# Performance work log

Measured on AMD Instinct MI355X. Metric: run time of the kernel, lower is better.

## Reference

```python
import jax, jax.numpy as jnp
import numpy as np

KS = 3                      # kernel side
GRID_SIZE = 5
SPLINE_ORDER = 3
N_CONVS = 8
IN_FEAT = KS * KS           # KANLinear in_features per patch
NCOEF = GRID_SIZE + SPLINE_ORDER  # number of B-spline basis functions


def setup_inputs() -> dict:
    key = jax.random.key(0)
    k1, k2, k3, k4 = jax.random.split(key, 4)
    x = jax.random.normal(k1, (8, 32, 64, 64), jnp.float32)
    # efficient-kan KANLinear params, stacked over the n_convs independent kernels
    base_weight = jax.random.normal(k2, (N_CONVS, IN_FEAT), jnp.float32) / np.sqrt(IN_FEAT).astype(np.float32)
    spline_weight = jax.random.normal(k3, (N_CONVS, IN_FEAT, NCOEF), jnp.float32) * 0.1
    spline_scaler = jax.random.normal(k4, (N_CONVS, IN_FEAT), jnp.float32) / np.sqrt(IN_FEAT).astype(np.float32)
    # knot grid: uniform over grid_range=[-1,1], extended by spline_order on each side
    h = 2.0 / GRID_SIZE
    g = jnp.arange(-SPLINE_ORDER, GRID_SIZE + SPLINE_ORDER + 1, dtype=jnp.float32) * h - 1.0
    grid = jnp.tile(g[None, :], (IN_FEAT, 1))  # [in, G+2k+1]
    return {"x": x, "base_weight": base_weight, "spline_weight": spline_weight,
            "spline_scaler": spline_scaler, "grid": grid}


def b_splines(x, grid):
    # x: [..., in], grid: [in, G+2k+1] -> bases [..., in, G+k]  (Cox-de Boor)
    xe = x[..., None]
    bases = ((xe >= grid[:, :-1]) & (xe < grid[:, 1:])).astype(x.dtype)
    for k in range(1, SPLINE_ORDER + 1):
        left = (xe - grid[:, :-(k + 1)]) / (grid[:, k:-1] - grid[:, :-(k + 1)])
        right = (grid[:, k + 1:] - xe) / (grid[:, k + 1:] - grid[:, 1:-k])
        bases = left * bases[..., :-1] + right * bases[..., 1:]
    return bases


def reference(x, base_weight, spline_weight, spline_scaler, grid):
    B, C, H, W = x.shape
    ho, wo = H - KS + 1, W - KS + 1  # stride 1, dilation 1, no padding
    # im2col: [B, C*KS*KS, ho, wo], channel-major feature order (matches torch Unfold)
    patches = jax.lax.conv_general_dilated_patches(x, (KS, KS), (1, 1), 'VALID')
    patches = patches.reshape(B, C, IN_FEAT, ho * wo).transpose(0, 1, 3, 2)  # [B,C,L,in]
    # KANLinear(out_features=1) applied per conv n over each patch
    base = jnp.einsum('bcli,ni->bcnl', jax.nn.silu(patches), base_weight)
    basis = b_splines(patches, grid)                     # [B,C,L,in,coef]
    sw = spline_weight * spline_scaler[..., None]        # scaled spline weight [n,in,coef]
    spl = jnp.einsum('bclis,nis->bcnl', basis, sw)
    # output channel index = kern + channel * n_convs (channel-major)
    return (base + spl).reshape(B, C * N_CONVS, ho, wo)
```

## Files before the change

kernel.cpp:

```cpp
#include <hip/hip_runtime.h>
#include <hip/hip_bf16.h>

#define N_CONVS 8
#define IN_FEAT 9
#define NCOEF 8
#define NKNOT 12
#define HH 64
#define WW 64
#define HO 62
#define WO 62
#define BAND 16
#define LROWS 18
#define LW 67


__global__ __launch_bounds__(704) void kan_prep(const float* __restrict__ bw,
                                                const float* __restrict__ sw,
                                                const float* __restrict__ sc,
                                                const float* __restrict__ grid,
                                                float* __restrict__ cbuf) {
    int t = threadIdx.x;
    if (t < 648) {
        int j = t % 9, ni = t / 9;
        cbuf[t] = (j == 0) ? bw[ni] : sw[ni * 8 + (j - 1)] * sc[ni];
    } else if (t < 659) {
        int j = t - 648; cbuf[t] = 1.0f / (grid[j + 1] - grid[j]);
    } else if (t < 669) {
        int j = t - 659; cbuf[t] = 1.0f / (grid[j + 2] - grid[j]);
    } else if (t < 678) {
        int j = t - 669; cbuf[t] = 1.0f / (grid[j + 3] - grid[j]);
    }
}

__global__ __launch_bounds__(256, 3) void kan_main(const float* __restrict__ x,
                                                   const float* __restrict__ grid,
                                                   const float* __restrict__ cbuf,
                                                   float* __restrict__ out) {
    __shared__ float feat[LROWS * LW * 9];

    const int blk  = blockIdx.x;
    const int band = blk & 3;
    const int img  = blk >> 2;
    const int r0   = band * BAND;
    const int nr       = (HO - r0) < BAND ? (HO - r0) : BAND;
    const int nrows_in = (HH - r0) < LROWS ? (HH - r0) : LROWS;

    float g[NKNOT];
#pragma unroll
    for (int j = 0; j < NKNOT; j++) g[j] = grid[j];
    float i1[11], i2[10], i3[9];
#pragma unroll
    for (int j = 0; j < 11; j++) i1[j] = cbuf[648 + j];
#pragma unroll
    for (int j = 0; j < 10; j++) i2[j] = cbuf[659 + j];
#pragma unroll
    for (int j = 0; j < 9; j++)  i3[j] = cbuf[669 + j];

    const float* xb = x + (size_t)img * (HH * WW) + (size_t)r0 * WW;
    for (int p = threadIdx.x; p < nrows_in * WW; p += 256) {
        const int r = p >> 6, c = p & 63;
        const float xv = xb[r * WW + c];

        const float sg = 1.0f / (1.0f + expf(-xv));
        const float s0 = xv * sg;

        float ee[12], d[12];
#pragma unroll
        for (int j = 0; j < 12; j++) {
            ee[j] = xv - g[j];
            d[j]  = (xv >= g[j]) ? 1.0f : 0.0f;
        }
        float b0[11];
#pragma unroll
        for (int j = 0; j < 11; j++) b0[j] = d[j] - d[j + 1];
        float b1[10];
#pragma unroll
        for (int j = 0; j < 10; j++)
            b1[j] = (ee[j] * i1[j]) * b0[j] - (ee[j + 2] * i1[j + 1]) * b0[j + 1];
        float b2[9];
#pragma unroll
        for (int j = 0; j < 9; j++)
            b2[j] = (ee[j] * i2[j]) * b1[j] - (ee[j + 3] * i2[j + 1]) * b1[j + 1];
        float b3[8];
#pragma unroll
        for (int j = 0; j < 8; j++)
            b3[j] = (ee[j] * i3[j]) * b2[j] - (ee[j + 4] * i3[j + 1]) * b2[j + 1];

        float* f = &feat[(r * LW + c) * 9];
        f[0] = s0;
#pragma unroll
        for (int j = 0; j < 8; j++) f[j + 1] = b3[j];
    }
    __syncthreads();

    const int row = threadIdx.x >> 4;
    const int xs  = (threadIdx.x & 15) * 4;
    if (row < nr) {
        float acc[N_CONVS][4];
#pragma unroll
        for (int n = 0; n < N_CONVS; n++)
#pragma unroll
            for (int t = 0; t < 4; t++) acc[n][t] = 0.0f;

#pragma unroll 1
        for (int ky = 0; ky < 3; ky++) {
            float fw[6][9];
#pragma unroll
            for (int c6 = 0; c6 < 6; c6++) {
                const float* fp = &feat[((row + ky) * LW + xs + c6) * 9];
#pragma unroll
                for (int j = 0; j < 9; j++) fw[c6][j] = fp[j];
            }
#pragma unroll
            for (int kx = 0; kx < 3; kx++) {
#pragma unroll
                for (int n = 0; n < N_CONVS; n++) {
#pragma unroll
                    for (int j = 0; j < 9; j++) {
                        const float w = cbuf[((n * 9) + (ky * 3 + kx)) * 9 + j];
#pragma unroll
                        for (int t = 0; t < 4; t++)
                            acc[n][t] = fmaf(fw[kx + t][j], w, acc[n][t]);
                    }
                }
            }
        }

        const int oy = r0 + row;
        float* ob = out + ((size_t)img * N_CONVS) * (HO * WO) + oy * WO + xs;
#pragma unroll
        for (int n = 0; n < N_CONVS; n++) {
            float* o = ob + n * (HO * WO);
            *(float2*)o = make_float2(acc[n][0], acc[n][1]);
            if (xs < 58) *(float2*)(o + 2) = make_float2(acc[n][2], acc[n][3]);
        }
    }
}

extern "C" void kernel_launch(void* const* d_in, const int* in_sizes, int n_in,
                              void* d_out, int out_size, void* d_ws, size_t ws_size,
                              hipStream_t stream) {
    const float* x    = (const float*)d_in[0];
    const float* bw   = (const float*)d_in[1];
    const float* sw   = (const float*)d_in[2];
    const float* sc   = (const float*)d_in[3];
    const float* grid = (const float*)d_in[4];
    float* out  = (float*)d_out;
    float* cbuf = (float*)d_ws;

    kan_prep<<<1, 704, 0, stream>>>(bw, sw, sc, grid, cbuf);
    kan_main<<<256 * 4, 256, 0, stream>>>(x, grid, cbuf, out);
}
```

Baseline: 95.48 us.

## Fuse weight prep into main kernel and use fast reciprocal/exp intrinsics

Removes the separate prep kernel launch by computing reciprocal knot spacings in-kernel and reading base/spline/scaler weights directly, applying the spline scaler once per (n,i) after the spline dot product. SiLU now uses __expf and hardware rcp instead of IEEE division, and the LDS row stride shrinks from 67 to 65. This saves a launch and its serialization, and trades some precision for cheaper transcendental work. The inner loop gains two extra FMAs per (n,i) group, and weights are now fetched as scalar loads from three arrays instead of one.

```diff
diff --git a/kernel.cpp b/kernel.cpp
--- a/kernel.cpp
+++ b/kernel.cpp
@@ -1,68 +1,50 @@
 #include <hip/hip_runtime.h>
 #include <hip/hip_bf16.h>
 
+
 #define N_CONVS 8
-#define IN_FEAT 9
-#define NCOEF 8
-#define NKNOT 12
 #define HH 64
 #define WW 64
 #define HO 62
 #define WO 62
 #define BAND 16
 #define LROWS 18
-#define LW 67
+#define LW 65
 
-
-__global__ __launch_bounds__(704) void kan_prep(const float* __restrict__ bw,
-                                                const float* __restrict__ sw,
-                                                const float* __restrict__ sc,
-                                                const float* __restrict__ grid,
-                                                float* __restrict__ cbuf) {
-    int t = threadIdx.x;
-    if (t < 648) {
-        int j = t % 9, ni = t / 9;
-        cbuf[t] = (j == 0) ? bw[ni] : sw[ni * 8 + (j - 1)] * sc[ni];
-    } else if (t < 659) {
-        int j = t - 648; cbuf[t] = 1.0f / (grid[j + 1] - grid[j]);
-    } else if (t < 669) {
-        int j = t - 659; cbuf[t] = 1.0f / (grid[j + 2] - grid[j]);
-    } else if (t < 678) {
-        int j = t - 669; cbuf[t] = 1.0f / (grid[j + 3] - grid[j]);
-    }
-}
-
-__global__ __launch_bounds__(256, 3) void kan_main(const float* __restrict__ x,
-                                                   const float* __restrict__ grid,
-                                                   const float* __restrict__ cbuf,
-                                                   float* __restrict__ out) {
+__global__ __launch_bounds__(256, 3) void kan_fused(
+    const float* __restrict__ x,
+    const float* __restrict__ bw,
+    const float* __restrict__ sw,
+    const float* __restrict__ sc,
+    const float* __restrict__ grid,
+    float* __restrict__ out)
+{
     __shared__ float feat[LROWS * LW * 9];
 
     const int blk  = blockIdx.x;
     const int band = blk & 3;
     const int img  = blk >> 2;
     const int r0   = band * BAND;
-    const int nr       = (HO - r0) < BAND ? (HO - r0) : BAND;
-    const int nrows_in = (HH - r0) < LROWS ? (HH - r0) : LROWS;
+    const int nr   = (HO - r0) < BAND ? (HO - r0) : BAND;
+    const int nin  = (HH - r0) < LROWS ? (HH - r0) : LROWS;
 
-    float g[NKNOT];
+    float g[12];
 #pragma unroll
-    for (int j = 0; j < NKNOT; j++) g[j] = grid[j];
+    for (int j = 0; j < 12; j++) g[j] = grid[j];
     float i1[11], i2[10], i3[9];
 #pragma unroll
-    for (int j = 0; j < 11; j++) i1[j] = cbuf[648 + j];
+    for (int j = 0; j < 11; j++) i1[j] = __builtin_amdgcn_rcpf(g[j + 1] - g[j]);
 #pragma unroll
-    for (int j = 0; j < 10; j++) i2[j] = cbuf[659 + j];
+    for (int j = 0; j < 10; j++) i2[j] = __builtin_amdgcn_rcpf(g[j + 2] - g[j]);
 #pragma unroll
-    for (int j = 0; j < 9; j++)  i3[j] = cbuf[669 + j];
+    for (int j = 0; j < 9; j++)  i3[j] = __builtin_amdgcn_rcpf(g[j + 3] - g[j]);
 
     const float* xb = x + (size_t)img * (HH * WW) + (size_t)r0 * WW;
-    for (int p = threadIdx.x; p < nrows_in * WW; p += 256) {
+    for (int p = threadIdx.x; p < nin * WW; p += 256) {
         const int r = p >> 6, c = p & 63;
-        const float xv = xb[r * WW + c];
+        const float xv = xb[p];
 
-        const float sg = 1.0f / (1.0f + expf(-xv));
-        const float s0 = xv * sg;
+        const float s0 = xv * __builtin_amdgcn_rcpf(1.0f + __expf(-xv));
 
         float ee[12], d[12];
 #pragma unroll
@@ -113,21 +95,33 @@
             }
 #pragma unroll
             for (int kx = 0; kx < 3; kx++) {
+                const int i = ky * 3 + kx;
 #pragma unroll
                 for (int n = 0; n < N_CONVS; n++) {
+                    const float scv = sc[n * 9 + i];
+                    const float bwv = bw[n * 9 + i];
+                    const float* swp = sw + ((n * 9 + i) << 3);
+                    float s[4];
 #pragma unroll
-                    for (int j = 0; j < 9; j++) {
-                        const float w = cbuf[((n * 9) + (ky * 3 + kx)) * 9 + j];
+                    for (int t = 0; t < 4; t++) s[t] = swp[0] * fw[kx + t][1];
+#pragma unroll
+                    for (int j = 1; j < 8; j++) {
+                        const float w = swp[j];
 #pragma unroll
                         for (int t = 0; t < 4; t++)
-                            acc[n][t] = fmaf(fw[kx + t][j], w, acc[n][t]);
+                            s[t] = fmaf(w, fw[kx + t][j + 1], s[t]);
+                    }
+#pragma unroll
+                    for (int t = 0; t < 4; t++) {
+                        acc[n][t] = fmaf(scv, s[t], acc[n][t]);
+                        acc[n][t] = fmaf(bwv, fw[kx + t][0], acc[n][t]);
                     }
                 }
             }
         }
 
         const int oy = r0 + row;
-        float* ob = out + ((size_t)img * N_CONVS) * (HO * WO) + oy * WO + xs;
+        float* ob = out + (size_t)img * N_CONVS * (HO * WO) + oy * WO + xs;
 #pragma unroll
         for (int n = 0; n < N_CONVS; n++) {
             float* o = ob + n * (HO * WO);
@@ -145,9 +139,7 @@
     const float* sw   = (const float*)d_in[2];
     const float* sc   = (const float*)d_in[3];
     const float* grid = (const float*)d_in[4];
-    float* out  = (float*)d_out;
-    float* cbuf = (float*)d_ws;
+    float* out = (float*)d_out;
 
-    kan_prep<<<1, 704, 0, stream>>>(bw, sw, sc, grid, cbuf);
-    kan_main<<<256 * 4, 256, 0, stream>>>(x, grid, cbuf, out);
+    kan_fused<<<256 * 4, 256, 0, stream>>>(x, bw, sw, sc, grid, out);
 }
```

After: 95.47 us. About the same (-0.0%).
